# Optimization experiments

Measured on AMD Instinct MI355X. Metric: run time of the kernel, lower is better.

Reference implementation:

```python
import jax, jax.numpy as jnp
import numpy as np


def setup_inputs() -> dict:
    key = jax.random.key(0)
    k_y, k_cb = jax.random.split(key)
    B, C, H, W = 8, 192, 64, 64
    G, K = 8, 512
    d = C // G  # 24
    y = jax.random.normal(k_y, (B, C, H, W), dtype=jnp.float32)
    codebooks = jax.random.normal(k_cb, (G, K, d), dtype=jnp.float32)
    return {"y": y, "codebooks": codebooks}


def reference(y, codebooks):
    # y: [B, C, H, W]; codebooks: [G, K, d] with C == G*d
    B, C, H, W = y.shape
    G, K, d = codebooks.shape
    # split channels into G groups of dim d -> vectors at each spatial pos
    x = y.reshape(B, G, d, H, W).transpose(0, 3, 4, 1, 2)  # [B,H,W,G,d]
    x2 = jnp.sum(x * x, axis=-1, keepdims=True)            # [B,H,W,G,1]
    e2 = jnp.sum(codebooks * codebooks, axis=-1)           # [G,K]
    xe = jnp.einsum('bhwgd,gkd->bhwgk', x, codebooks)      # [B,H,W,G,K]
    dist = x2 - 2.0 * xe + e2                              # [B,H,W,G,K]
    idx = jnp.argmin(dist, axis=-1)                        # [B,H,W,G] int
    # gather quantized vectors per group (to_feather)
    q = codebooks[jnp.arange(G), idx]                      # [B,H,W,G,d]
    y_ba = q.transpose(0, 3, 4, 1, 2).reshape(B, C, H, W)  # [B,C,H,W]
    code_index = idx.transpose(0, 3, 1, 2)                 # [B,G,H,W]
    # straight-through estimator
    universal_ctx = y + jax.lax.stop_gradient(y_ba - y)
    return universal_ctx, y_ba, code_index[:, None]        # [B,1,G,H,W]
```

## Files before the change

### kernel.cpp

```cpp
#include <hip/hip_runtime.h>

#define B_   8
#define C_   192
#define HW_  4096
#define G_   8
#define K_   512
#define D_   24
#define CBSZ (K_ * D_)
#define THREADS 256
#define TILES_PER_BLOCK 16

typedef float  f32x4 __attribute__((ext_vector_type(4)));
typedef short  s16x8 __attribute__((ext_vector_type(8)));
typedef short  s16x4 __attribute__((ext_vector_type(4)));
typedef unsigned long long u64;

static __device__ __forceinline__ unsigned umin_(unsigned a, unsigned b){return a<b?a:b;}
static __device__ __forceinline__ unsigned umax_(unsigned a, unsigned b){return a>b?a:b;}
static __device__ __forceinline__ unsigned short f2bf(float x){
    unsigned u=__float_as_uint(x);
    return (unsigned short)((u + 0x7FFFu + ((u>>16)&1u))>>16);
}
static __device__ __forceinline__ float bf2f(unsigned short h){return __uint_as_float(((unsigned)h)<<16);}

__global__ __launch_bounds__(THREADS, 4) void vq_mfma2(
    const float* __restrict__ y, const float* __restrict__ cb, float* __restrict__ out)
{
    __shared__ unsigned short sB[32 * 512];

    const int bid = blockIdx.x;
    const int g = bid & 7;
    const int chunk = bid >> 3;
    const int tid = threadIdx.x;
    const int wave = tid >> 6, lane = tid & 63;
    const int c = lane & 15, q = lane >> 4;

    const float* cbg = cb + (size_t)g * CBSZ;

    {
        const f32x4* cb4 = (const f32x4*)cbg;
        for (int i = tid; i < CBSZ/4; i += THREADS) {
            f32x4 v = cb4[i];
            int i4 = i << 2;
            int n  = i4 / 24;
            int k0 = i4 - n * 24;
            int off = (n >> 4) * 512 + (((k0 >> 3) << 4) + (n & 15)) * 8 + (k0 & 7);
            s16x4 h;
            h[0]=(short)f2bf(v[0]); h[1]=(short)f2bf(v[1]);
            h[2]=(short)f2bf(v[2]); h[3]=(short)f2bf(v[3]);
            *(s16x4*)(&sB[off]) = h;
        }
        for (int n = tid; n < K_; n += THREADS) {
            const float* row = cbg + n * D_;
            double s = 0.0;
            #pragma unroll
            for (int j = 0; j < D_; ++j) { double v = (double)row[j]; s = fma(v,v,s); }
            unsigned short ehi = f2bf((float)s);
            unsigned short elo = f2bf((float)(s - (double)bf2f(ehi)));
            unsigned* dst = (unsigned*)(&sB[(n >> 4) * 512 + (48 + (n & 15)) * 8]);
            dst[0] = (unsigned)ehi | ((unsigned)elo << 16);
            dst[1] = 0u; dst[2] = 0u; dst[3] = 0u;
        }
    }
    __syncthreads();

    float* out0 = out;
    float* out1 = out + (size_t)(B_*C_)*HW_;
    float* out2 = out + (size_t)(2*B_*C_)*HW_;

    for (int mt = wave; mt < TILES_PER_BLOCK; mt += 4) {
        const int posT = chunk * 256 + mt * 16;
        const int bimg = posT >> 12;
        const int hw   = posT & (HW_-1);
        const size_t ybase = ((size_t)bimg*C_ + g*D_)*HW_ + hw;

        s16x8 Ah = {0,0,0,0,0,0,0,0}, Al = {0,0,0,0,0,0,0,0};
        if (q < 3) {
            #pragma unroll
            for (int j = 0; j < 8; ++j) {
                float xv = -2.0f * y[ybase + (size_t)(q*8+j)*HW_ + c];
                unsigned short hb = f2bf(xv);
                Ah[j] = (short)hb;
                Al[j] = (short)f2bf(xv - bf2f(hb));
            }
        } else {
            Ah[0] = (short)0x3F80; Ah[1] = (short)0x3F80;
        }

        unsigned b1[4], b2[4];
        #pragma unroll
        for (int r=0;r<4;++r){ b1[r]=0xFFFFFFFFu; b2[r]=0xFFFFFFFFu; }

        #pragma unroll 8
        for (int t = 0; t < 32; ++t) {
            s16x8 bh = *(const s16x8*)(&sB[t*512 + lane*8]);
            f32x4 acc = {256.0f, 256.0f, 256.0f, 256.0f};
            acc = __builtin_amdgcn_mfma_f32_16x16x32_bf16(Ah, bh, acc, 0,0,0);
            acc = __builtin_amdgcn_mfma_f32_16x16x32_bf16(Al, bh, acc, 0,0,0);
            #pragma unroll
            for (int r=0;r<4;++r){
                unsigned key = (__float_as_uint(acc[r]) & 0xFFFFFFE0u) | (unsigned)t;
                b2[r] = umin_(umax_(b1[r], key), b2[r]);
                b1[r] = umin_(b1[r], key);
            }
        }

        unsigned u1[4],u2[4],u3[4];
        #pragma unroll
        for (int r=0;r<4;++r){
            u1[r] = (b1[r] & 0xFFFFFE00u) | (((b1[r]&31u)<<4) | (unsigned)c);
            u2[r] = (b2[r] & 0xFFFFFE00u) | (((b2[r]&31u)<<4) | (unsigned)c);
            u3[r] = 0xFFFFFFFFu;
        }
        #pragma unroll
        for (int d=1; d<16; d<<=1){
            #pragma unroll
            for (int r=0;r<4;++r){
                unsigned o1=__shfl_xor(u1[r],d,64), o2=__shfl_xor(u2[r],d,64), o3=__shfl_xor(u3[r],d,64);
                unsigned x = umax_(u1[r],o1);
                unsigned yv= umin_(u2[r],o2);
                unsigned w = umax_(u2[r],o2);
                unsigned z = umin_(u3[r],o3);
                u1[r]=umin_(u1[r],o1);
                u2[r]=umin_(x,yv);
                u3[r]=umin_(umax_(x,yv), umin_(w,z));
            }
        }

        const int rr = c >> 2, cand = c & 3, row = (q<<2) + rr;
        unsigned s1v = (rr==0)?u1[0]:(rr==1)?u1[1]:(rr==2)?u1[2]:u1[3];
        unsigned s2v = (rr==0)?u2[0]:(rr==1)?u2[1]:(rr==2)?u2[2]:u2[3];
        unsigned s3v = (rr==0)?u3[0]:(rr==1)?u3[1]:(rr==2)?u3[2]:u3[3];
        unsigned sel = (cand==0)?s1v:(cand==1)?s2v:s3v;
        int kc = (int)(sel & 511u);

        const f32x4* ce4 = (const f32x4*)(cbg + kc * D_);
        float ef[24];
        #pragma unroll
        for (int v=0; v<6; ++v) *(f32x4*)&ef[v*4] = ce4[v];
        double s = 256.0;
        #pragma unroll
        for (int j=0;j<24;++j){
            double ev = (double)ef[j];
            double xv = -2.0 * (double)y[ybase + (size_t)j*HW_ + row];
            s = fma(ev, ev, s);
            s = fma(xv, ev, s);
        }
        u64 key64 = (((u64)__double_as_longlong(s)) & ~0x1FFull) | (u64)kc;
        if (cand == 3) key64 = ~0ull;
        u64 o = __shfl_xor(key64, 1, 64); key64 = o < key64 ? o : key64;
        o = __shfl_xor(key64, 2, 64);     key64 = o < key64 ? o : key64;
        int kwin = (int)(key64 & 511ull);

        const int p = c;
        const int srcl = ((p>>2)<<4) | ((p&3)<<2);
        int kw = __shfl(kwin, srcl, 64);
        const float* cw = cbg + kw * D_;
        #pragma unroll
        for (int i=0;i<6;++i){
            int ch = i*4 + q;
            float val = cw[ch];
            size_t oo = ybase + (size_t)ch*HW_ + p;
            out0[oo] = val;
            out1[oo] = val;
        }
        if (lane < 16)
            out2[((size_t)bimg*G_ + g)*HW_ + hw + lane] = (float)kw;
    }
}

extern "C" void kernel_launch(void* const* d_in, const int* in_sizes, int n_in,
                              void* d_out, int out_size, void* d_ws, size_t ws_size,
                              hipStream_t stream) {
    const float* y  = (const float*)d_in[0];
    const float* cb = (const float*)d_in[1];
    float* out = (float*)d_out;

    const int nblocks = 128 * G_;
    vq_mfma2<<<dim3(nblocks), dim3(THREADS), 0, stream>>>(y, cb, out);
}
```

Measured before the change: 121.2 us.

## Halve tiles per block, raise occupancy, use 32-bit indexing and split FP64 reductions

Cuts tiles per block from 16 to 8 and doubles the grid so more blocks are in flight, and raises the launch-bounds occupancy hint to 5. Swaps size_t address arithmetic for 32-bit ints and truncates the high bf16 part instead of rounding it. Splits the serial FP64 FMA chains for codebook norms and rescoring into independent accumulators to shorten dependency latency. The cost is that each block rebuilds the shared codebook tile over half as much work, doubling that setup overhead, and summation order changes slightly.

```diff
diff --git a/kernel.cpp b/kernel.cpp
--- a/kernel.cpp
+++ b/kernel.cpp
@@ -8,7 +8,7 @@
 #define D_   24
 #define CBSZ (K_ * D_)
 #define THREADS 256
-#define TILES_PER_BLOCK 16
+#define TILES_PER_BLOCK 8
 
 typedef float  f32x4 __attribute__((ext_vector_type(4)));
 typedef short  s16x8 __attribute__((ext_vector_type(8)));
@@ -23,7 +23,7 @@
 }
 static __device__ __forceinline__ float bf2f(unsigned short h){return __uint_as_float(((unsigned)h)<<16);}
 
-__global__ __launch_bounds__(THREADS, 4) void vq_mfma2(
+__global__ __launch_bounds__(THREADS, 5) void vq_mfma3(
     const float* __restrict__ y, const float* __restrict__ cb, float* __restrict__ out)
 {
     __shared__ unsigned short sB[32 * 512];
@@ -35,7 +35,7 @@
     const int wave = tid >> 6, lane = tid & 63;
     const int c = lane & 15, q = lane >> 4;
 
-    const float* cbg = cb + (size_t)g * CBSZ;
+    const float* cbg = cb + g * CBSZ;
 
     {
         const f32x4* cb4 = (const f32x4*)cbg;
@@ -52,9 +52,13 @@
         }
         for (int n = tid; n < K_; n += THREADS) {
             const float* row = cbg + n * D_;
-            double s = 0.0;
+            double s0 = 0.0, s1 = 0.0;
             #pragma unroll
-            for (int j = 0; j < D_; ++j) { double v = (double)row[j]; s = fma(v,v,s); }
+            for (int j = 0; j < D_; j += 2) {
+                double v0 = (double)row[j], v1 = (double)row[j+1];
+                s0 = fma(v0,v0,s0); s1 = fma(v1,v1,s1);
+            }
+            double s = s0 + s1;
             unsigned short ehi = f2bf((float)s);
             unsigned short elo = f2bf((float)(s - (double)bf2f(ehi)));
             unsigned* dst = (unsigned*)(&sB[(n >> 4) * 512 + (48 + (n & 15)) * 8]);
@@ -65,23 +69,24 @@
     __syncthreads();
 
     float* out0 = out;
-    float* out1 = out + (size_t)(B_*C_)*HW_;
-    float* out2 = out + (size_t)(2*B_*C_)*HW_;
+    float* out1 = out + B_*C_*HW_;
+    float* out2 = out + 2*B_*C_*HW_;
 
     for (int mt = wave; mt < TILES_PER_BLOCK; mt += 4) {
-        const int posT = chunk * 256 + mt * 16;
+        const int posT = chunk * (TILES_PER_BLOCK*16) + mt * 16;
         const int bimg = posT >> 12;
         const int hw   = posT & (HW_-1);
-        const size_t ybase = ((size_t)bimg*C_ + g*D_)*HW_ + hw;
+        const int ybase = (bimg*C_ + g*D_)*HW_ + hw;
+        const float* yb = y + ybase;
 
         s16x8 Ah = {0,0,0,0,0,0,0,0}, Al = {0,0,0,0,0,0,0,0};
         if (q < 3) {
             #pragma unroll
             for (int j = 0; j < 8; ++j) {
-                float xv = -2.0f * y[ybase + (size_t)(q*8+j)*HW_ + c];
-                unsigned short hb = f2bf(xv);
-                Ah[j] = (short)hb;
-                Al[j] = (short)f2bf(xv - bf2f(hb));
+                float xv = -2.0f * yb[(q*8+j)*HW_ + c];
+                unsigned u = __float_as_uint(xv);
+                Ah[j] = (short)(u >> 16);
+                Al[j] = (short)f2bf(xv - __uint_as_float(u & 0xFFFF0000u));
             }
         } else {
             Ah[0] = (short)0x3F80; Ah[1] = (short)0x3F80;
@@ -138,14 +143,21 @@
         float ef[24];
         #pragma unroll
         for (int v=0; v<6; ++v) *(f32x4*)&ef[v*4] = ce4[v];
-        double s = 256.0;
+        double a0=0.0, a1=0.0, a2=0.0, a3=0.0;
         #pragma unroll
-        for (int j=0;j<24;++j){
-            double ev = (double)ef[j];
-            double xv = -2.0 * (double)y[ybase + (size_t)j*HW_ + row];
-            s = fma(ev, ev, s);
-            s = fma(xv, ev, s);
+        for (int j=0;j<24;j+=4){
+            double e0=(double)ef[j],   e1=(double)ef[j+1];
+            double e2=(double)ef[j+2], e3=(double)ef[j+3];
+            double x0=-2.0*(double)yb[j*HW_ + row];
+            double x1=-2.0*(double)yb[(j+1)*HW_ + row];
+            double x2=-2.0*(double)yb[(j+2)*HW_ + row];
+            double x3=-2.0*(double)yb[(j+3)*HW_ + row];
+            a0 = fma(e0, e0+x0, a0);
+            a1 = fma(e1, e1+x1, a1);
+            a2 = fma(e2, e2+x2, a2);
+            a3 = fma(e3, e3+x3, a3);
         }
+        double s = ((a0 + a1) + (a2 + a3)) + 256.0;
         u64 key64 = (((u64)__double_as_longlong(s)) & ~0x1FFull) | (u64)kc;
         if (cand == 3) key64 = ~0ull;
         u64 o = __shfl_xor(key64, 1, 64); key64 = o < key64 ? o : key64;
@@ -160,12 +172,12 @@
         for (int i=0;i<6;++i){
             int ch = i*4 + q;
             float val = cw[ch];
-            size_t oo = ybase + (size_t)ch*HW_ + p;
+            int oo = ybase + ch*HW_ + p;
             out0[oo] = val;
             out1[oo] = val;
         }
         if (lane < 16)
-            out2[((size_t)bimg*G_ + g)*HW_ + hw + lane] = (float)kw;
+            out2[(bimg*G_ + g)*HW_ + hw + lane] = (float)kw;
     }
 }
 
@@ -176,6 +188,6 @@
     const float* cb = (const float*)d_in[1];
     float* out = (float*)d_out;
 
-    const int nblocks = 128 * G_;
-    vq_mfma2<<<dim3(nblocks), dim3(THREADS), 0, stream>>>(y, cb, out);
+    const int nblocks = 256 * G_;
+    vq_mfma3<<<dim3(nblocks), dim3(THREADS), 0, stream>>>(y, cb, out);
 }
```

Result: no change. 122.8 us (+1.3%).
